# Kernel optimization log

Measured on AMD Instinct MI355X. Metric: run time of the kernel, lower is better.

## Reference

```python
import jax, jax.numpy as jnp
import numpy as np

N = 16384          # points in the (single-batch) cloud
K = 16             # boundary_k
C = 20             # num semantic classes (ScanNet-style)
IGNORE = -1        # ignore_index
BOUNDARY_W = 1.0   # boundary_loss_weight


def setup_inputs() -> dict:
    key = jax.random.key(0)
    k1, k2, k3 = jax.random.split(key, 3)
    coord = jax.random.normal(k1, (N, 3), jnp.float32)
    seg_logits = jax.random.normal(k2, (N, C), jnp.float32)
    segment = jax.random.randint(k3, (N,), 0, C, dtype=jnp.int32)
    return {"coord": coord, "seg_logits": seg_logits, "segment": segment, "offset": N}


def _knn_idx(coord):
    # brute-force kNN (loop=False): exclude self via +inf diagonal
    d2 = jnp.sum(coord * coord, axis=1)                       # [N]
    dist = d2[:, None] + d2[None, :] - 2.0 * (coord @ coord.T)  # [N, N]
    dist = dist + jnp.where(jnp.eye(dist.shape[0], dtype=bool), jnp.inf, 0.0)
    _, idx = jax.lax.top_k(-dist, K)                          # [N, K] neighbor (src) indices per center (dst)
    return idx


def _masked_ce(logp_tgt, mask):
    # mean cross-entropy over masked points (matches torch reduction='mean' w/ ignore_index)
    cnt = jnp.sum(mask)
    s = jnp.sum(jnp.where(mask, logp_tgt, 0.0))
    return jnp.where(cnt > 0, -s / jnp.maximum(cnt, 1).astype(logp_tgt.dtype), 0.0)


def reference(coord, seg_logits, segment, offset):
    # --- boundary mask: knn_graph -> per-edge label diff -> scatter-max to dst ---
    nbr = _knn_idx(coord)                                     # [N, K] src indices, dst = row index
    nbr_seg = segment[nbr]                                    # gather: [N, K]
    valid_pt = segment != IGNORE                              # [N]
    valid = (nbr_seg != IGNORE) & valid_pt[:, None]           # per-edge valid
    diff = valid & (nbr_seg != segment[:, None])              # per-edge label mismatch
    boundary = jnp.any(diff, axis=1)                          # scatter-max over dst == row-wise any

    # --- main loss: cross-entropy with ignore_index ---
    logp = jax.nn.log_softmax(seg_logits, axis=-1)            # [N, C]
    tgt = jnp.clip(segment, 0, C - 1)
    logp_tgt = jnp.take_along_axis(logp, tgt[:, None], axis=1)[:, 0]  # [N]
    main_loss = _masked_ce(logp_tgt, valid_pt)

    # --- boundary loss: CE restricted to boundary points (0 if none) ---
    bmask = boundary & valid_pt
    boundary_loss = _masked_ce(logp_tgt, bmask)

    loss = main_loss + BOUNDARY_W * boundary_loss
    return loss
```

## Files before the change

kernel.cpp:

```cpp
#include <hip/hip_runtime.h>
#include <hip/hip_bf16.h>
#include <math.h>

#define N_PTS 16384
#define KNN   16
#define NCLS  20
#define BND_W 1.0f

#define THREADS 512
#define WAVES   8
#define RPW     32
#define RPB     (WAVES * RPW)
#define RBLKS   (N_PTS / RPB)
#define CSPLIT  16
#define CAND_PB (N_PTS / CSPLIT)
#define CHUNK   512
#define NCHUNK  (CAND_PB / CHUNK)

typedef short  short8 __attribute__((ext_vector_type(8)));
typedef float  f32x4  __attribute__((ext_vector_type(4)));

__device__ __forceinline__ unsigned short f2bf(float x) {
    union { __hip_bfloat16 h; unsigned short u; } cv;
    cv.h = __float2bfloat16(x);
    return cv.u;
}
__device__ __forceinline__ float bf2f(unsigned short b) {
    union { __hip_bfloat16 h; unsigned short u; } cv;
    cv.u = b;
    return __bfloat162float(cv.h);
}

__device__ __forceinline__ void build_b(const float* __restrict__ coord,
                                        const int* __restrict__ seg, int j,
                                        unsigned short* out) {
    float x = coord[3 * j], y = coord[3 * j + 1], z = coord[3 * j + 2];
    int lab = seg[j];
    unsigned short xh = f2bf(x), yh = f2bf(y), zh = f2bf(z);
    unsigned short xl = f2bf(x - bf2f(xh));
    unsigned short yl = f2bf(y - bf2f(yh));
    unsigned short zl = f2bf(z - bf2f(zh));
    float h = 0.5f * fmaf(x, x, fmaf(y, y, z * z));
    unsigned short hh = f2bf(h);
    unsigned short hl = f2bf(h - bf2f(hh));
    out[0] = xh; out[1] = xh; out[2] = xl;
    out[3] = yh; out[4] = yh; out[5] = yl;
    out[6] = zh; out[7] = zh; out[8] = zl;
    out[9]  = hh ^ 0x8000u;
    out[10] = hl ^ 0x8000u;
#pragma unroll
    for (int s = 0; s < NCLS; s++) out[11 + s] = (lab == s) ? 0x3F80u : 0u;
    out[31] = (lab < 0) ? 0x3F80u : 0u;
}

template<bool PASS1>
__device__ __forceinline__ void build_a(const float* __restrict__ coord,
                                        const int* __restrict__ seg, int i,
                                        unsigned short* out) {
    float x = coord[3 * i], y = coord[3 * i + 1], z = coord[3 * i + 2];
    int lab = seg[i];
    unsigned short xh = f2bf(x), yh = f2bf(y), zh = f2bf(z);
    unsigned short xl = f2bf(x - bf2f(xh));
    unsigned short yl = f2bf(y - bf2f(yh));
    unsigned short zl = f2bf(z - bf2f(zh));
    out[0] = xh; out[1] = xl; out[2] = xh;
    out[3] = yh; out[4] = yl; out[5] = yh;
    out[6] = zh; out[7] = zl; out[8] = zh;
    out[9] = 0x3F80u; out[10] = 0x3F80u;
    const unsigned short nb = 0xC480u;
#pragma unroll
    for (int s = 0; s < NCLS; s++) out[11 + s] = (PASS1 && lab == s) ? nb : 0u;
    out[31] = PASS1 ? nb : 0u;
}

template<bool PASS1>
__global__ __launch_bounds__(THREADS, 6) void k_pass(const float* __restrict__ coord,
                                                     const int* __restrict__ seg,
                                                     float* __restrict__ smax_part,
                                                     int* __restrict__ cnt_part,
                                                     float* __restrict__ accum,
                                                     unsigned* __restrict__ done) {
    __shared__ __align__(16) unsigned short smem[CHUNK * 32];
    __shared__ float thr_lds[RPB];
    const int tid  = threadIdx.x;
    const int lane = tid & 63, wave = tid >> 6;
    const int l15  = lane & 15, l4 = lane >> 4;
    const int rb   = blockIdx.x * RPB;
    const int split = blockIdx.y;
    const int cb   = split * CAND_PB;

    if (PASS1 && blockIdx.x == 0 && split == 0 && tid == 0) {
        accum[0] = 0.f; accum[1] = 0.f; accum[2] = 0.f; accum[3] = 0.f;
        *done = 0u;
    }

    if (!PASS1 && tid < RPB) {
        int row = rb + tid;
        float m = smax_part[row];
#pragma unroll
        for (int s = 1; s < CSPLIT; s++) m = fmaxf(m, smax_part[s * N_PTS + row]);
        thr_lds[tid] = m;
    }

    if (tid < RPB) build_a<PASS1>(coord, seg, rb + tid, &smem[tid * 32]);
    __syncthreads();
    short8 af0, af1;
    {
        const short8* ap = (const short8*)smem;
        int r0 = wave * RPW + l15;
        af0 = ap[r0 * 4 + l4];
        af1 = ap[(r0 + 16) * 4 + l4];
    }
    float thr0[4], thr1[4];
    if (!PASS1) {
#pragma unroll
        for (int r = 0; r < 4; r++) {
            thr0[r] = thr_lds[wave * RPW + l4 * 4 + r];
            thr1[r] = thr_lds[wave * RPW + 16 + l4 * 4 + r];
        }
    }
    __syncthreads();

    f32x4 rmax0, rmax1;
    int cv0[4], cv1[4];
#pragma unroll
    for (int r = 0; r < 4; r++) {
        rmax0[r] = -3.0e38f; rmax1[r] = -3.0e38f;
        cv0[r] = 0; cv1[r] = 0;
    }

    const short8* bp = (const short8*)smem;
    const int bidx = l15 * 4 + (l4 ^ ((l15 >> 1) & 3));
    const f32x4 zero = {0.f, 0.f, 0.f, 0.f};

    for (int cc = 0; cc < NCHUNK; cc++) {
        {
            __attribute__((aligned(16))) unsigned short be[32];
            build_b(coord, seg, cb + cc * CHUNK + tid, be);
            short8* wp = (short8*)smem;
            int swz = (tid >> 1) & 3;
#pragma unroll
            for (int kb = 0; kb < 4; kb++)
                wp[tid * 4 + (kb ^ swz)] = ((const short8*)be)[kb];
        }
        __syncthreads();

#pragma unroll 4
        for (int c0 = 0; c0 < CHUNK; c0 += 32) {
            short8 bA = bp[bidx + c0 * 4];
            short8 bB = bp[bidx + (c0 + 16) * 4];
            f32x4 dA0 = __builtin_amdgcn_mfma_f32_16x16x32_bf16(af0, bA, zero, 0, 0, 0);
            f32x4 dA1 = __builtin_amdgcn_mfma_f32_16x16x32_bf16(af1, bA, zero, 0, 0, 0);
            f32x4 dB0 = __builtin_amdgcn_mfma_f32_16x16x32_bf16(af0, bB, zero, 0, 0, 0);
            f32x4 dB1 = __builtin_amdgcn_mfma_f32_16x16x32_bf16(af1, bB, zero, 0, 0, 0);
            if (PASS1) {
#pragma unroll
                for (int r = 0; r < 4; r++) {
                    rmax0[r] = fmaxf(fmaxf(rmax0[r], dA0[r]), dB0[r]);
                    rmax1[r] = fmaxf(fmaxf(rmax1[r], dA1[r]), dB1[r]);
                }
            } else {
#pragma unroll
                for (int r = 0; r < 4; r++) {
                    cv0[r] += ((dA0[r] > thr0[r]) ? 1 : 0) + ((dB0[r] > thr0[r]) ? 1 : 0);
                    cv1[r] += ((dA1[r] > thr1[r]) ? 1 : 0) + ((dB1[r] > thr1[r]) ? 1 : 0);
                }
            }
        }
        __syncthreads();
    }

    const int row0 = rb + wave * RPW + l4 * 4;
    if (PASS1) {
#pragma unroll
        for (int m = 1; m < 16; m <<= 1)
#pragma unroll
            for (int r = 0; r < 4; r++) {
                rmax0[r] = fmaxf(rmax0[r], __shfl_xor(rmax0[r], m, 64));
                rmax1[r] = fmaxf(rmax1[r], __shfl_xor(rmax1[r], m, 64));
            }
        if (l15 == 0) {
#pragma unroll
            for (int r = 0; r < 4; r++) {
                smax_part[split * N_PTS + row0 + r]      = rmax0[r];
                smax_part[split * N_PTS + row0 + 16 + r] = rmax1[r];
            }
        }
    } else {
#pragma unroll
        for (int m = 1; m < 16; m <<= 1)
#pragma unroll
            for (int r = 0; r < 4; r++) {
                cv0[r] += __shfl_xor(cv0[r], m, 64);
                cv1[r] += __shfl_xor(cv1[r], m, 64);
            }
        if (l15 == 0) {
#pragma unroll
            for (int r = 0; r < 4; r++) {
                cnt_part[split * N_PTS + row0 + r]      = cv0[r];
                cnt_part[split * N_PTS + row0 + 16 + r] = cv1[r];
            }
        }
    }
}

__device__ __forceinline__ float waveReduceSum(float v) {
#pragma unroll
    for (int off = 32; off > 0; off >>= 1) v += __shfl_down(v, off, 64);
    return v;
}

__global__ __launch_bounds__(256) void k_ce(const float* __restrict__ logits,
                                            const int* __restrict__ seg,
                                            const int* __restrict__ cnt_part,
                                            float* __restrict__ accum,
                                            unsigned* __restrict__ done,
                                            float* __restrict__ out) {
    const int i = blockIdx.x * 256 + threadIdx.x;
    float s_main = 0.f, n_main = 0.f, s_bnd = 0.f, n_bnd = 0.f;
    {
        int s = seg[i];
        bool valid = (s != -1);
        const float4* row4 = (const float4*)(logits + (size_t)i * NCLS);
        float a[NCLS];
        float4 v0 = row4[0], v1 = row4[1], v2 = row4[2], v3 = row4[3], v4 = row4[4];
        a[0]=v0.x; a[1]=v0.y; a[2]=v0.z; a[3]=v0.w;
        a[4]=v1.x; a[5]=v1.y; a[6]=v1.z; a[7]=v1.w;
        a[8]=v2.x; a[9]=v2.y; a[10]=v2.z; a[11]=v2.w;
        a[12]=v3.x; a[13]=v3.y; a[14]=v3.z; a[15]=v3.w;
        a[16]=v4.x; a[17]=v4.y; a[18]=v4.z; a[19]=v4.w;
        float m = a[0];
#pragma unroll
        for (int c = 1; c < NCLS; c++) m = fmaxf(m, a[c]);
        float se = 0.f;
#pragma unroll
        for (int c = 0; c < NCLS; c++) se += __expf(a[c] - m);
        int tgt = min(max(s, 0), NCLS - 1);
        float at = 0.f;
#pragma unroll
        for (int c = 0; c < NCLS; c++) at += (c == tgt) ? a[c] : 0.f;
        float logp = at - m - __logf(se);
        int cnt = 0;
#pragma unroll
        for (int sp = 0; sp < CSPLIT; sp++) cnt += cnt_part[sp * N_PTS + i];
        bool bnd = valid && ((cnt - 1) < KNN);
        if (valid) { s_main = logp; n_main = 1.f; }
        if (bnd)   { s_bnd  = logp; n_bnd  = 1.f; }
    }
    s_main = waveReduceSum(s_main);
    n_main = waveReduceSum(n_main);
    s_bnd  = waveReduceSum(s_bnd);
    n_bnd  = waveReduceSum(n_bnd);
    if ((threadIdx.x & 63) == 0) {
        atomicAdd(&accum[0], s_main);
        atomicAdd(&accum[1], n_main);
        atomicAdd(&accum[2], s_bnd);
        atomicAdd(&accum[3], n_bnd);
    }
    __syncthreads();
    if (threadIdx.x == 0) {
        __threadfence();
        unsigned old = atomicAdd(done, 1u);
        if (old == gridDim.x - 1) {
            float sm = atomicAdd(&accum[0], 0.f);
            float cm = atomicAdd(&accum[1], 0.f);
            float sb = atomicAdd(&accum[2], 0.f);
            float cb = atomicAdd(&accum[3], 0.f);
            float main_loss = (cm > 0.f) ? (-sm / fmaxf(cm, 1.f)) : 0.f;
            float bnd_loss  = (cb > 0.f) ? (-sb / fmaxf(cb, 1.f)) : 0.f;
            out[0] = main_loss + BND_W * bnd_loss;
        }
    }
}

extern "C" void kernel_launch(void* const* d_in, const int* in_sizes, int n_in,
                              void* d_out, int out_size, void* d_ws, size_t ws_size,
                              hipStream_t stream) {
    const float* coord  = (const float*)d_in[0];
    const float* logits = (const float*)d_in[1];
    const int*   seg    = (const int*)d_in[2];
    (void)in_sizes; (void)n_in; (void)out_size; (void)ws_size;

    float*    smax_part = (float*)d_ws;
    int*      cnt_part  = (int*)((char*)d_ws + CSPLIT * N_PTS * 4);
    float*    accum     = (float*)((char*)d_ws + 2 * CSPLIT * N_PTS * 4);
    unsigned* done      = (unsigned*)((char*)d_ws + 2 * CSPLIT * N_PTS * 4 + 16);

    dim3 grid(RBLKS, CSPLIT);
    k_pass<true> <<<grid, THREADS, 0, stream>>>(coord, seg, smax_part, cnt_part, accum, done);
    k_pass<false><<<grid, THREADS, 0, stream>>>(coord, seg, smax_part, cnt_part, accum, done);
    k_ce         <<<N_PTS / 256, 256, 0, stream>>>(logits, seg, cnt_part, accum, done, (float*)d_out);
}
```

Baseline: 64.33 us.

## Precompute bf16 A/B encodings once and stream B tiles into LDS directly

Adds a small encode kernel that writes the split-bf16 A and B operand rows (coordinates, norm term, one-hot labels) to workspace once, instead of rebuilding them in every block of both passes. The pass kernels then copy B chunks into LDS with global_load_lds and load A fragments straight from global memory, masking the label columns in pass 2. The candidate split drops from 16 to 8 and the chunk grows from 512 to 1024, which halves the number of per-row partials and occupancy is lowered to 4. The cost is an extra launch, more workspace traffic and larger LDS use per block, which may reduce how many blocks fit per CU.

```diff
diff --git a/kernel.cpp b/kernel.cpp
--- a/kernel.cpp
+++ b/kernel.cpp
@@ -12,9 +12,9 @@
 #define RPW     32
 #define RPB     (WAVES * RPW)
 #define RBLKS   (N_PTS / RPB)
-#define CSPLIT  16
+#define CSPLIT  8
 #define CAND_PB (N_PTS / CSPLIT)
-#define CHUNK   512
+#define CHUNK   1024
 #define NCHUNK  (CAND_PB / CHUNK)
 
 typedef short  short8 __attribute__((ext_vector_type(8)));
@@ -31,11 +31,21 @@
     return __bfloat162float(cv.h);
 }
 
-__device__ __forceinline__ void build_b(const float* __restrict__ coord,
-                                        const int* __restrict__ seg, int j,
-                                        unsigned short* out) {
-    float x = coord[3 * j], y = coord[3 * j + 1], z = coord[3 * j + 2];
-    int lab = seg[j];
+__device__ __forceinline__ void gload16(const void* g, void* l) {
+    __builtin_amdgcn_global_load_lds(
+        (const __attribute__((address_space(1))) unsigned int*)g,
+        (__attribute__((address_space(3))) unsigned int*)l, 16, 0, 0);
+}
+
+__global__ __launch_bounds__(THREADS) void k_enc(const float* __restrict__ coord,
+                                                 const int* __restrict__ seg,
+                                                 unsigned short* __restrict__ aenc,
+                                                 unsigned short* __restrict__ benc,
+                                                 float* __restrict__ accum,
+                                                 unsigned* __restrict__ done) {
+    const int i = blockIdx.x * THREADS + threadIdx.x;
+    float x = coord[3 * i], y = coord[3 * i + 1], z = coord[3 * i + 2];
+    int lab = seg[i];
     unsigned short xh = f2bf(x), yh = f2bf(y), zh = f2bf(z);
     unsigned short xl = f2bf(x - bf2f(xh));
     unsigned short yl = f2bf(y - bf2f(yh));
@@ -43,43 +53,43 @@
     float h = 0.5f * fmaf(x, x, fmaf(y, y, z * z));
     unsigned short hh = f2bf(h);
     unsigned short hl = f2bf(h - bf2f(hh));
-    out[0] = xh; out[1] = xh; out[2] = xl;
-    out[3] = yh; out[4] = yh; out[5] = yl;
-    out[6] = zh; out[7] = zh; out[8] = zl;
-    out[9]  = hh ^ 0x8000u;
-    out[10] = hl ^ 0x8000u;
-#pragma unroll
-    for (int s = 0; s < NCLS; s++) out[11 + s] = (lab == s) ? 0x3F80u : 0u;
-    out[31] = (lab < 0) ? 0x3F80u : 0u;
+    const unsigned short one = 0x3F80u, nb = 0xC480u;
+
+    __attribute__((aligned(16))) unsigned short a[32], b[32];
+    a[0] = xh; a[1] = xl; a[2] = xh;
+    a[3] = yh; a[4] = yl; a[5] = yh;
+    a[6] = zh; a[7] = zl; a[8] = zh;
+    a[9] = one; a[10] = one;
+#pragma unroll
+    for (int s = 0; s < NCLS; s++) a[11 + s] = (lab == s) ? nb : 0u;
+    a[31] = nb;
+
+    b[0] = xh; b[1] = xh; b[2] = xl;
+    b[3] = yh; b[4] = yh; b[5] = yl;
+    b[6] = zh; b[7] = zh; b[8] = zl;
+    b[9]  = hh ^ 0x8000u;
+    b[10] = hl ^ 0x8000u;
+#pragma unroll
+    for (int s = 0; s < NCLS; s++) b[11 + s] = (lab == s) ? one : 0u;
+    b[31] = (lab < 0) ? one : 0u;
+
+    short8* ap = (short8*)(aenc + (size_t)i * 32);
+#pragma unroll
+    for (int kb = 0; kb < 4; kb++) ap[kb] = ((const short8*)a)[kb];
+    short8* bp = (short8*)(benc + (size_t)i * 32);
+    const int swz = (i >> 1) & 3;
+#pragma unroll
+    for (int kb = 0; kb < 4; kb++) bp[kb ^ swz] = ((const short8*)b)[kb];
+
+    if (i < 4) accum[i] = 0.f;
+    if (i == 4) *done = 0u;
 }
 
 template<bool PASS1>
-__device__ __forceinline__ void build_a(const float* __restrict__ coord,
-                                        const int* __restrict__ seg, int i,
-                                        unsigned short* out) {
-    float x = coord[3 * i], y = coord[3 * i + 1], z = coord[3 * i + 2];
-    int lab = seg[i];
-    unsigned short xh = f2bf(x), yh = f2bf(y), zh = f2bf(z);
-    unsigned short xl = f2bf(x - bf2f(xh));
-    unsigned short yl = f2bf(y - bf2f(yh));
-    unsigned short zl = f2bf(z - bf2f(zh));
-    out[0] = xh; out[1] = xl; out[2] = xh;
-    out[3] = yh; out[4] = yl; out[5] = yh;
-    out[6] = zh; out[7] = zl; out[8] = zh;
-    out[9] = 0x3F80u; out[10] = 0x3F80u;
-    const unsigned short nb = 0xC480u;
-#pragma unroll
-    for (int s = 0; s < NCLS; s++) out[11 + s] = (PASS1 && lab == s) ? nb : 0u;
-    out[31] = PASS1 ? nb : 0u;
-}
-
-template<bool PASS1>
-__global__ __launch_bounds__(THREADS, 6) void k_pass(const float* __restrict__ coord,
-                                                     const int* __restrict__ seg,
+__global__ __launch_bounds__(THREADS, 4) void k_pass(const unsigned short* __restrict__ aenc,
+                                                     const unsigned short* __restrict__ benc,
                                                      float* __restrict__ smax_part,
-                                                     int* __restrict__ cnt_part,
-                                                     float* __restrict__ accum,
-                                                     unsigned* __restrict__ done) {
+                                                     int* __restrict__ cnt_part) {
     __shared__ __align__(16) unsigned short smem[CHUNK * 32];
     __shared__ float thr_lds[RPB];
     const int tid  = threadIdx.x;
@@ -89,9 +99,12 @@
     const int split = blockIdx.y;
     const int cb   = split * CAND_PB;
 
-    if (PASS1 && blockIdx.x == 0 && split == 0 && tid == 0) {
-        accum[0] = 0.f; accum[1] = 0.f; accum[2] = 0.f; accum[3] = 0.f;
-        *done = 0u;
+    {
+        const char* gsrc = (const char*)benc + (size_t)cb * 64;
+#pragma unroll
+        for (int r = 0; r < 8; r++)
+            gload16(gsrc + (wave * 8 + r) * 1024 + lane * 16,
+                    (char*)smem + (wave * 8 + r) * 1024);
     }
 
     if (!PASS1 && tid < RPB) {
@@ -102,15 +115,24 @@
         thr_lds[tid] = m;
     }
 
-    if (tid < RPB) build_a<PASS1>(coord, seg, rb + tid, &smem[tid * 32]);
+    const int r0 = rb + wave * RPW + l15;
+    short8 af0 = *(const short8*)(aenc + (size_t)r0 * 32 + l4 * 8);
+    short8 af1 = *(const short8*)(aenc + (size_t)(r0 + 16) * 32 + l4 * 8);
+    if (!PASS1) {
+        union { short8 s; unsigned u[4]; } c0v, c1v;
+        c0v.s = af0; c1v.s = af1;
+        if (l4 == 1) {
+            c0v.u[1] &= 0x0000FFFFu; c0v.u[2] = 0u; c0v.u[3] = 0u;
+            c1v.u[1] &= 0x0000FFFFu; c1v.u[2] = 0u; c1v.u[3] = 0u;
+        } else if (l4 >= 2) {
+            c0v.u[0] = c0v.u[1] = c0v.u[2] = c0v.u[3] = 0u;
+            c1v.u[0] = c1v.u[1] = c1v.u[2] = c1v.u[3] = 0u;
+        }
+        af0 = c0v.s; af1 = c1v.s;
+    }
+
     __syncthreads();
-    short8 af0, af1;
-    {
-        const short8* ap = (const short8*)smem;
-        int r0 = wave * RPW + l15;
-        af0 = ap[r0 * 4 + l4];
-        af1 = ap[(r0 + 16) * 4 + l4];
-    }
+
     float thr0[4], thr1[4];
     if (!PASS1) {
 #pragma unroll
@@ -119,7 +141,6 @@
             thr1[r] = thr_lds[wave * RPW + 16 + l4 * 4 + r];
         }
     }
-    __syncthreads();
 
     f32x4 rmax0, rmax1;
     int cv0[4], cv1[4];
@@ -134,17 +155,6 @@
     const f32x4 zero = {0.f, 0.f, 0.f, 0.f};
 
     for (int cc = 0; cc < NCHUNK; cc++) {
-        {
-            __attribute__((aligned(16))) unsigned short be[32];
-            build_b(coord, seg, cb + cc * CHUNK + tid, be);
-            short8* wp = (short8*)smem;
-            int swz = (tid >> 1) & 3;
-#pragma unroll
-            for (int kb = 0; kb < 4; kb++)
-                wp[tid * 4 + (kb ^ swz)] = ((const short8*)be)[kb];
-        }
-        __syncthreads();
-
 #pragma unroll 4
         for (int c0 = 0; c0 < CHUNK; c0 += 32) {
             short8 bA = bp[bidx + c0 * 4];
@@ -167,7 +177,15 @@
                 }
             }
         }
-        __syncthreads();
+        if (cc + 1 < NCHUNK) {
+            __syncthreads();
+            const char* gsrc = (const char*)benc + (size_t)(cb + (cc + 1) * CHUNK) * 64;
+#pragma unroll
+            for (int r = 0; r < 8; r++)
+                gload16(gsrc + (wave * 8 + r) * 1024 + lane * 16,
+                        (char*)smem + (wave * 8 + r) * 1024);
+            __syncthreads();
+        }
     }
 
     const int row0 = rb + wave * RPW + l4 * 4;
@@ -281,13 +299,16 @@
     const int*   seg    = (const int*)d_in[2];
     (void)in_sizes; (void)n_in; (void)out_size; (void)ws_size;
 
-    float*    smax_part = (float*)d_ws;
-    int*      cnt_part  = (int*)((char*)d_ws + CSPLIT * N_PTS * 4);
-    float*    accum     = (float*)((char*)d_ws + 2 * CSPLIT * N_PTS * 4);
-    unsigned* done      = (unsigned*)((char*)d_ws + 2 * CSPLIT * N_PTS * 4 + 16);
+    unsigned short* aenc = (unsigned short*)d_ws;
+    unsigned short* benc = (unsigned short*)((char*)d_ws + (1u << 20));
+    float* smax_part = (float*)((char*)d_ws + (2u << 20));
+    int*   cnt_part  = (int*)((char*)d_ws + (2u << 20) + (512u << 10));
+    float* accum     = (float*)((char*)d_ws + (3u << 20));
+    unsigned* done   = (unsigned*)((char*)d_ws + (3u << 20) + 16);
 
     dim3 grid(RBLKS, CSPLIT);
-    k_pass<true> <<<grid, THREADS, 0, stream>>>(coord, seg, smax_part, cnt_part, accum, done);
-    k_pass<false><<<grid, THREADS, 0, stream>>>(coord, seg, smax_part, cnt_part, accum, done);
+    k_enc        <<<N_PTS / THREADS, THREADS, 0, stream>>>(coord, seg, aenc, benc, accum, done);
+    k_pass<true> <<<grid, THREADS, 0, stream>>>(aenc, benc, smax_part, cnt_part);
+    k_pass<false><<<grid, THREADS, 0, stream>>>(aenc, benc, smax_part, cnt_part);
     k_ce         <<<N_PTS / 256, 256, 0, stream>>>(logits, seg, cnt_part, accum, done, (float*)d_out);
 }
```

Measured after the change: 64.96 us. About the same (+1.0%).
